# Kernel optimization log

Measured on AMD Instinct MI355X. Metric: run time of the kernel, lower is better.

The kernel has to match this reference:

```python
import jax, jax.numpy as jnp
import numpy as np

CLIP = 100000.0


def heaviside(x):
    # smooth heaviside surrogate used by the layer
    return (jnp.tanh(10.0 * x) + 1.0) * 0.5


def evapotranspiration(wu, wl, wd, pet):
    et1 = heaviside(wu - pet) * pet + heaviside(pet - wu) * wu
    rem = heaviside(0.0 - (pet - et1)) * 0.0 + heaviside(pet - et1) * (pet - et1)
    et22 = heaviside(rem - wl) * wl + heaviside(wl - rem) * rem
    et2 = heaviside(rem) * et22
    et33 = heaviside(rem - et2 - wd) * wd + heaviside(wd - (rem - et2)) * (rem - et2)
    et3 = heaviside(rem - et2) * et33
    return et1, et2, et3


def runoff_production(wu, wl, wd, p, wum, wlm, wdm, b, c):
    wum = wum * 19.9 + 0.1
    wlm = wlm * 30.0 + 60.0
    wdm = wdm * 60.0 + 60.0
    c = c * 0.19 + 0.01
    b = b * 0.3 + 0.1
    w_total = wum + wlm + wdm
    s = c * (wu / w_total) ** 2 + b * (wl / w_total) ** 2
    return heaviside(p - s) * (p - s)


def water_source_partition(runoff, k1, k2, k3):
    k1 = k1 * 0.69 + 0.01
    k2 = k2 * 0.69 + 0.01
    k3 = k3 * 0.89 + 0.01
    surface = k1 * runoff
    interflow = k2 * (runoff - surface)
    baseflow = k3 * (runoff - surface - interflow)
    return surface, interflow, baseflow


def flow_routing(surface, interflow, baseflow):
    return surface + 0.5 * interflow + 0.25 * baseflow


def xaj_forward(inputs, wum, wlm, wdm, c, b, k1, k2, k3):
    # inputs: (B, T, 3) channels = [pet, tmean, p]
    pet_seq = inputs[:, :, 0:1]
    p_seq = inputs[:, :, 2:3]

    B = inputs.shape[0]
    # time-major driver: (T, B, 2) = [pet, p] per step (tmean unused in step)
    xs = jnp.moveaxis(jnp.stack([inputs[:, :, 0], inputs[:, :, 2]], axis=-1), 1, 0)

    def step(state, xt):
        # state: (B, 3) = [wu, wl, wd]; xt: (B, 2) = [pet, p]
        wu, wl, wd = state[:, 0], state[:, 1], state[:, 2]
        pet, p = xt[:, 0], xt[:, 1]
        et1, et2, et3 = evapotranspiration(wu, wl, wd, pet)
        wu_n = wu + jnp.clip(p - et1, -CLIP, CLIP)
        wl_n = wl + jnp.clip(p - et1 - et2, -CLIP, CLIP)
        wd_n = wd + jnp.clip(p - et1 - et2 - et3, -CLIP, CLIP)
        ns = jnp.stack([wu_n, wl_n, wd_n], axis=1)
        return ns, ns

    init = jnp.zeros((B, 3), dtype=inputs.dtype)
    _, traj = jax.lax.scan(step, init, xs)           # (T, B, 3)
    outputs = jnp.moveaxis(traj, 0, 1)               # (B, T, 3)

    wu = outputs[:, :, 0:1]
    wl = outputs[:, :, 1:2]
    wd = outputs[:, :, 2:3]

    # NOTE: original call site passes (wu, wd, wl, ...) and (wum, wdm, wlm, ...)
    # positionally into runoff_production -- replicated faithfully.
    runoff = runoff_production(wu, wd, wl, p_seq, wum, wdm, wlm, b, c)
    surface, interflow, baseflow = water_source_partition(runoff, k1, k2, k3)
    total_q = flow_routing(surface, interflow, baseflow)  # (B, T, 1)
    return total_q


def setup_inputs() -> dict:
    key = jax.random.key(0)
    ks = jax.random.split(key, 9)
    B, T = 4096, 2048
    inp = {"inputs": jax.random.uniform(ks[0], (B, T, 3), dtype=jnp.float32)}
    for i, name in enumerate(["wum", "wlm", "wdm", "c", "b", "k1", "k2", "k3"]):
        inp[name] = jax.random.uniform(ks[i + 1], (1,), dtype=jnp.float32)
    return inp


def reference(inputs, wum, wlm, wdm, c, b, k1, k2, k3):
    return xaj_forward(inputs, wum, wlm, wdm, c, b, k1, k2, k3)
```

## Files before the change

### kernel.cpp

```cpp
#include <hip/hip_runtime.h>

typedef float  f32x4 __attribute__((ext_vector_type(4)));
typedef __fp16 f16x2 __attribute__((ext_vector_type(2)));

#define T_LEN 2048
#define GROUP 32
#define NG    (T_LEN / GROUP)
#define NT    (NG + 3)
#define KH    28.853901f

__device__ __forceinline__ float hs_neg(float z) {
    float e = __builtin_amdgcn_exp2f(z);
    return __builtin_amdgcn_rcpf(1.0f + e);
}

#define WAITV(N) asm volatile("s_waitcnt vmcnt(" #N ")" ::: "memory")
#define WAITL()  asm volatile("s_waitcnt lgkmcnt(0)" ::: "memory")
#define TICK_BARRIER() do {                                   \
    asm volatile("s_waitcnt lgkmcnt(0)" ::: "memory");        \
    __builtin_amdgcn_s_barrier();                             \
    __builtin_amdgcn_sched_barrier(0); } while (0)

#define DMA_CHUNK(SLOT, C) do {                                                \
    const float* g_ = row + (size_t)(C) * 48;                                  \
    _Pragma("unroll")                                                          \
    for (int j_ = 0; j_ < 12; ++j_) {                                          \
        __builtin_amdgcn_global_load_lds(                                      \
            (const __attribute__((address_space(1))) void*)(g_ + 4 * j_),      \
            (__attribute__((address_space(3))) void*)&s_in[SLOT][j_][0],       \
            16, 0, 0);                                                         \
    } } while (0)

__global__ __launch_bounds__(256, 1)
void xaj_k32_kernel(const float* __restrict__ inp,
                    const float* __restrict__ p_wum,
                    const float* __restrict__ p_wlm,
                    const float* __restrict__ p_wdm,
                    const float* __restrict__ p_c,
                    const float* __restrict__ p_b,
                    const float* __restrict__ p_k1,
                    const float* __restrict__ p_k2,
                    const float* __restrict__ p_k3,
                    float* __restrict__ out)
{
    __shared__ f32x4        s_in  [3][12][64];
    __shared__ float        s_krem[2][GROUP][64];
    __shared__ float        s_kd1 [2][GROUP][64];
    __shared__ float        s_ku  [2][GROUP][64];
    __shared__ float        s_kd2 [2][GROUP][64];
    __shared__ float        s_kwd [2][GROUP][64];
    __shared__ unsigned int s_wup [4][GROUP][64];

    const int lane  = threadIdx.x & 63;
    const int wv    = threadIdx.x >> 6;
    const int chain = blockIdx.x * 64 + lane;
    const float* __restrict__ row = inp + (size_t)chain * (3 * T_LEN);
    float* __restrict__ orow      = out + (size_t)chain * T_LEN;

    const float wum = p_wum[0], wlm = p_wlm[0], wdm = p_wdm[0];
    const float cc  = p_c[0],   bb  = p_b[0];
    const float k1  = p_k1[0],  k2  = p_k2[0],  k3 = p_k3[0];

    const float w_total = (wum * 19.9f + 0.1f)
                        + (wdm * 30.0f + 60.0f)
                        + (wlm * 60.0f + 60.0f);
    const float inv_wt = 1.0f / w_total;
    const float c_s = cc * 0.19f + 0.01f;
    const float b_s = bb * 0.3f  + 0.1f;
    const float k1s = k1 * 0.69f + 0.01f;
    const float k2s = k2 * 0.69f + 0.01f;
    const float k3s = k3 * 0.89f + 0.01f;
    const float Kq = k1s + 0.5f * k2s * (1.0f - k1s)
                   + 0.25f * k3s * (1.0f - k1s) * (1.0f - k2s);
    const float C1 = inv_wt / KH;

    float Kst = 0.0f;
    int s0 = 0, s1 = 1, s2 = 2;

    if (wv == 0) { DMA_CHUNK(0, 0); DMA_CHUNK(1, 1); }

#pragma clang loop unroll(disable)
    for (int T = 0; T < NT; ++T) {
        if (wv == 0) {
            if (T < NG) {
                const int g = T;
                WAITV(0);
                f32x4 fv[24];
#pragma unroll
                for (int j = 0; j < 12; ++j) fv[j]      = s_in[s0][j][lane];
#pragma unroll
                for (int j = 0; j < 12; ++j) fv[12 + j] = s_in[s1][j][lane];
                WAITL();
                __builtin_amdgcn_sched_barrier(0);
                const int c2 = 2 * g + 2, c3 = 2 * g + 3;
                if (c2 < 2 * NG) DMA_CHUNK(s2, c2);
                if (c3 < 2 * NG) DMA_CHUNK(s0, c3);
                float Kwu = Kst;
#pragma unroll
                for (int j = 0; j < GROUP; ++j) {
                    const int k0 = 3 * j, k2i = 3 * j + 2;
                    float pet = fv[k0 >> 2][k0 & 3];
                    float p   = fv[k2i >> 2][k2i & 3];
                    float KHpet = KH * pet, Kp = KH * p;
                    float arg  = KHpet - Kwu;
                    float a    = hs_neg(arg);
                    float Kwun = fmaf(-arg, a, Kp);
                    float Kd1  = Kwun - Kwu;
                    float Ky   = arg + (Kwun - Kp);
                    float hx   = hs_neg(-Ky);
                    float Krem = hx * Ky;
                    s_krem[g & 1][j][lane] = Krem;
                    s_kd1 [g & 1][j][lane] = Kd1;
                    f16x2 pk = __builtin_amdgcn_cvt_pkrtz(Kwun, p);
                    s_wup[g & 3][j][lane] = __builtin_bit_cast(unsigned int, pk);
                    Kwu = Kwun;
                }
                Kst = Kwu;
                int t0 = s0; s0 = s2; s2 = s1; s1 = t0;
            }
        } else if (wv == 1) {
            if (T >= 1 && T <= NG) {
                const int g = T - 1;
                float Kwl = Kst;
#pragma unroll
                for (int j = 0; j < GROUP; ++j) {
                    float Krem = s_krem[g & 1][j][lane];
                    float Kd1  = s_kd1 [g & 1][j][lane];
                    float hrem = hs_neg(-Krem);
                    float S    = Kwl + Kd1;
                    float A    = fmaf(-hrem, Krem, S);
                    float arg  = Kwl - Krem;
                    float b2   = hs_neg(arg);
                    float harg = hrem * arg;
                    float Kwln = fmaf(-b2, harg, A);
                    float Ket2 = S - Kwln;
                    s_ku [g & 1][j][lane] = Krem - Ket2;
                    s_kd2[g & 1][j][lane] = Kd1 - Ket2;
                    Kwl = Kwln;
                }
                Kst = Kwl;
            }
        } else if (wv == 2) {
            if (T >= 2 && T <= NG + 1) {
                const int g = T - 2;
                float Kwd = Kst;
#pragma unroll
                for (int j = 0; j < GROUP; ++j) {
                    float Ku  = s_ku [g & 1][j][lane];
                    float Kd2 = s_kd2[g & 1][j][lane];
                    float hu  = hs_neg(-Ku);
                    float S2  = Kwd + Kd2;
                    float A2  = fmaf(-hu, Ku, S2);
                    float arg = Kwd - Ku;
                    float c2v = hs_neg(arg);
                    float harg = hu * arg;
                    float Kwdn = fmaf(-c2v, harg, A2);
                    s_kwd[g & 1][j][lane] = Kwdn;
                    Kwd = Kwdn;
                }
                Kst = Kwd;
            }
        } else {
            if (T >= 3) {
                const int g = T - 3;
                float qv[GROUP];
#pragma unroll
                for (int j = 0; j < GROUP; ++j) {
                    unsigned int pw = s_wup[g & 3][j][lane];
                    f16x2 pk = __builtin_bit_cast(f16x2, pw);
                    float Kwu_ = (float)pk[0];
                    float p    = (float)pk[1];
                    float Kwd_ = s_kwd[g & 1][j][lane];
                    float ru = Kwu_ * C1;
                    float rd = Kwd_ * C1;
                    float s2v = fmaf(c_s * ru, ru, (b_s * rd) * rd);
                    float ps = p - s2v;
                    float so = hs_neg(-KH * ps);
                    qv[j] = ps * so * Kq;
                }
                f32x4* o4 = (f32x4*)(orow + (size_t)g * GROUP);
#pragma unroll
                for (int i = 0; i < GROUP / 4; ++i) {
                    f32x4 q = {qv[4*i], qv[4*i+1], qv[4*i+2], qv[4*i+3]};
                    o4[i] = q;
                }
            }
        }
        TICK_BARRIER();
    }
}

extern "C" void kernel_launch(void* const* d_in, const int* in_sizes, int n_in,
                              void* d_out, int out_size, void* d_ws, size_t ws_size,
                              hipStream_t stream) {
    const float* inp = (const float*)d_in[0];
    const int B = out_size / T_LEN;
    dim3 block(256), grid(B / 64);
    xaj_k32_kernel<<<grid, block, 0, stream>>>(
        inp,
        (const float*)d_in[1],
        (const float*)d_in[2],
        (const float*)d_in[3],
        (const float*)d_in[4],
        (const float*)d_in[5],
        (const float*)d_in[6],
        (const float*)d_in[7],
        (const float*)d_in[8],
        (float*)d_out);
}
```

Baseline: 134.4 us.

## Run two 4-wave stage pipelines per block with smaller groups and fp16 wd handoff

Each 512-thread block now holds two independent 4-wave pipelines, each serving 64 chains, so there are half as many blocks. The time group shrinks from 32 to 16 steps and the input prefetch is simplified to a double buffer. The wd trajectory handed to the output wave is stored in fp16 to save LDS. The aim is more chains resident per CU and better latency hiding across the serial recurrence stages. The cost is twice as many barrier ticks, fewer blocks across the GPU, and reduced precision on the stored wd value.

```diff
diff --git a/kernel.cpp b/kernel.cpp
--- a/kernel.cpp
+++ b/kernel.cpp
@@ -4,7 +4,7 @@
 typedef __fp16 f16x2 __attribute__((ext_vector_type(2)));
 
 #define T_LEN 2048
-#define GROUP 32
+#define GROUP 16
 #define NG    (T_LEN / GROUP)
 #define NT    (NG + 3)
 #define KH    28.853901f
@@ -21,39 +21,41 @@
     __builtin_amdgcn_s_barrier();                             \
     __builtin_amdgcn_sched_barrier(0); } while (0)
 
-#define DMA_CHUNK(SLOT, C) do {                                                \
-    const float* g_ = row + (size_t)(C) * 48;                                  \
+#define DMA_GROUP(PIPE, SLOT, G) do {                                          \
+    const float* g_ = row + (size_t)(G) * 48;                                  \
     _Pragma("unroll")                                                          \
     for (int j_ = 0; j_ < 12; ++j_) {                                          \
         __builtin_amdgcn_global_load_lds(                                      \
             (const __attribute__((address_space(1))) void*)(g_ + 4 * j_),      \
-            (__attribute__((address_space(3))) void*)&s_in[SLOT][j_][0],       \
+            (__attribute__((address_space(3))) void*)&s_in[PIPE][SLOT][j_][0], \
             16, 0, 0);                                                         \
     } } while (0)
 
-__global__ __launch_bounds__(256, 1)
-void xaj_k32_kernel(const float* __restrict__ inp,
-                    const float* __restrict__ p_wum,
-                    const float* __restrict__ p_wlm,
-                    const float* __restrict__ p_wdm,
-                    const float* __restrict__ p_c,
-                    const float* __restrict__ p_b,
-                    const float* __restrict__ p_k1,
-                    const float* __restrict__ p_k2,
-                    const float* __restrict__ p_k3,
-                    float* __restrict__ out)
+__global__ __launch_bounds__(512, 1)
+void xaj_dual_kernel(const float* __restrict__ inp,
+                     const float* __restrict__ p_wum,
+                     const float* __restrict__ p_wlm,
+                     const float* __restrict__ p_wdm,
+                     const float* __restrict__ p_c,
+                     const float* __restrict__ p_b,
+                     const float* __restrict__ p_k1,
+                     const float* __restrict__ p_k2,
+                     const float* __restrict__ p_k3,
+                     float* __restrict__ out)
 {
-    __shared__ f32x4        s_in  [3][12][64];
-    __shared__ float        s_krem[2][GROUP][64];
-    __shared__ float        s_kd1 [2][GROUP][64];
-    __shared__ float        s_ku  [2][GROUP][64];
-    __shared__ float        s_kd2 [2][GROUP][64];
-    __shared__ float        s_kwd [2][GROUP][64];
-    __shared__ unsigned int s_wup [4][GROUP][64];
+    __shared__ f32x4        s_in  [2][2][12][64];
+    __shared__ float        s_krem[2][2][GROUP][64];
+    __shared__ float        s_kd1 [2][2][GROUP][64];
+    __shared__ float        s_ku  [2][2][GROUP][64];
+    __shared__ float        s_kd2 [2][2][GROUP][64];
+    __shared__ __fp16       s_kwd [2][2][GROUP][64];
+    __shared__ unsigned int s_wup [2][4][GROUP][64];
 
     const int lane  = threadIdx.x & 63;
     const int wv    = threadIdx.x >> 6;
-    const int chain = blockIdx.x * 64 + lane;
+    const int pipe  = wv >> 2;
+    const int stage = wv & 3;
+    const int chain = blockIdx.x * 128 + pipe * 64 + lane;
     const float* __restrict__ row = inp + (size_t)chain * (3 * T_LEN);
     float* __restrict__ orow      = out + (size_t)chain * T_LEN;
 
@@ -75,26 +77,21 @@
     const float C1 = inv_wt / KH;
 
     float Kst = 0.0f;
-    int s0 = 0, s1 = 1, s2 = 2;
-
-    if (wv == 0) { DMA_CHUNK(0, 0); DMA_CHUNK(1, 1); }
+
+    if (stage == 0) DMA_GROUP(pipe, 0, 0);
 
 #pragma clang loop unroll(disable)
     for (int T = 0; T < NT; ++T) {
-        if (wv == 0) {
+        if (stage == 0) {
             if (T < NG) {
                 const int g = T;
                 WAITV(0);
-                f32x4 fv[24];
-#pragma unroll
-                for (int j = 0; j < 12; ++j) fv[j]      = s_in[s0][j][lane];
-#pragma unroll
-                for (int j = 0; j < 12; ++j) fv[12 + j] = s_in[s1][j][lane];
+                f32x4 fv[12];
+#pragma unroll
+                for (int j = 0; j < 12; ++j) fv[j] = s_in[pipe][g & 1][j][lane];
                 WAITL();
                 __builtin_amdgcn_sched_barrier(0);
-                const int c2 = 2 * g + 2, c3 = 2 * g + 3;
-                if (c2 < 2 * NG) DMA_CHUNK(s2, c2);
-                if (c3 < 2 * NG) DMA_CHUNK(s0, c3);
+                if (g + 1 < NG) DMA_GROUP(pipe, (g + 1) & 1, g + 1);
                 float Kwu = Kst;
 #pragma unroll
                 for (int j = 0; j < GROUP; ++j) {
@@ -109,23 +106,23 @@
                     float Ky   = arg + (Kwun - Kp);
                     float hx   = hs_neg(-Ky);
                     float Krem = hx * Ky;
-                    s_krem[g & 1][j][lane] = Krem;
-                    s_kd1 [g & 1][j][lane] = Kd1;
+                    s_krem[pipe][g & 1][j][lane] = Krem;
+                    s_kd1 [pipe][g & 1][j][lane] = Kd1;
                     f16x2 pk = __builtin_amdgcn_cvt_pkrtz(Kwun, p);
-                    s_wup[g & 3][j][lane] = __builtin_bit_cast(unsigned int, pk);
+                    s_wup[pipe][g & 3][j][lane] =
+                        __builtin_bit_cast(unsigned int, pk);
                     Kwu = Kwun;
                 }
                 Kst = Kwu;
-                int t0 = s0; s0 = s2; s2 = s1; s1 = t0;
-            }
-        } else if (wv == 1) {
+            }
+        } else if (stage == 1) {
             if (T >= 1 && T <= NG) {
                 const int g = T - 1;
                 float Kwl = Kst;
 #pragma unroll
                 for (int j = 0; j < GROUP; ++j) {
-                    float Krem = s_krem[g & 1][j][lane];
-                    float Kd1  = s_kd1 [g & 1][j][lane];
+                    float Krem = s_krem[pipe][g & 1][j][lane];
+                    float Kd1  = s_kd1 [pipe][g & 1][j][lane];
                     float hrem = hs_neg(-Krem);
                     float S    = Kwl + Kd1;
                     float A    = fmaf(-hrem, Krem, S);
@@ -134,20 +131,20 @@
                     float harg = hrem * arg;
                     float Kwln = fmaf(-b2, harg, A);
                     float Ket2 = S - Kwln;
-                    s_ku [g & 1][j][lane] = Krem - Ket2;
-                    s_kd2[g & 1][j][lane] = Kd1 - Ket2;
+                    s_ku [pipe][g & 1][j][lane] = Krem - Ket2;
+                    s_kd2[pipe][g & 1][j][lane] = Kd1 - Ket2;
                     Kwl = Kwln;
                 }
                 Kst = Kwl;
             }
-        } else if (wv == 2) {
+        } else if (stage == 2) {
             if (T >= 2 && T <= NG + 1) {
                 const int g = T - 2;
                 float Kwd = Kst;
 #pragma unroll
                 for (int j = 0; j < GROUP; ++j) {
-                    float Ku  = s_ku [g & 1][j][lane];
-                    float Kd2 = s_kd2[g & 1][j][lane];
+                    float Ku  = s_ku [pipe][g & 1][j][lane];
+                    float Kd2 = s_kd2[pipe][g & 1][j][lane];
                     float hu  = hs_neg(-Ku);
                     float S2  = Kwd + Kd2;
                     float A2  = fmaf(-hu, Ku, S2);
@@ -155,7 +152,7 @@
                     float c2v = hs_neg(arg);
                     float harg = hu * arg;
                     float Kwdn = fmaf(-c2v, harg, A2);
-                    s_kwd[g & 1][j][lane] = Kwdn;
+                    s_kwd[pipe][g & 1][j][lane] = (__fp16)Kwdn;
                     Kwd = Kwdn;
                 }
                 Kst = Kwd;
@@ -166,11 +163,11 @@
                 float qv[GROUP];
 #pragma unroll
                 for (int j = 0; j < GROUP; ++j) {
-                    unsigned int pw = s_wup[g & 3][j][lane];
+                    unsigned int pw = s_wup[pipe][g & 3][j][lane];
                     f16x2 pk = __builtin_bit_cast(f16x2, pw);
                     float Kwu_ = (float)pk[0];
                     float p    = (float)pk[1];
-                    float Kwd_ = s_kwd[g & 1][j][lane];
+                    float Kwd_ = (float)s_kwd[pipe][g & 1][j][lane];
                     float ru = Kwu_ * C1;
                     float rd = Kwd_ * C1;
                     float s2v = fmaf(c_s * ru, ru, (b_s * rd) * rd);
@@ -195,8 +192,8 @@
                               hipStream_t stream) {
     const float* inp = (const float*)d_in[0];
     const int B = out_size / T_LEN;
-    dim3 block(256), grid(B / 64);
-    xaj_k32_kernel<<<grid, block, 0, stream>>>(
+    dim3 block(512), grid(B / 128);
+    xaj_dual_kernel<<<grid, block, 0, stream>>>(
         inp,
         (const float*)d_in[1],
         (const float*)d_in[2],
```

After: 202.3 us. 50.5% more time.

## Move input loading to the output wave and halve the group size

Applied to the files above, without the earlier changes.

Input DMA and unpacking move from the first recurrence wave to the fourth (output) wave, which pre-scales pet and p into a shared buffer one group ahead. This keeps the serial wave-0 chain free of load latency. Group size drops from 32 to 16, doubling the number of barrier ticks but shortening each pipeline stage. Pairs of intermediates are packed into float2 LDS stores, and the deep-store value is kept in fp16, which costs precision in the runoff computation.

```diff
diff --git a/kernel.cpp b/kernel.cpp
--- a/kernel.cpp
+++ b/kernel.cpp
@@ -1,10 +1,11 @@
 #include <hip/hip_runtime.h>
 
+typedef float  f32x2 __attribute__((ext_vector_type(2)));
 typedef float  f32x4 __attribute__((ext_vector_type(4)));
 typedef __fp16 f16x2 __attribute__((ext_vector_type(2)));
 
 #define T_LEN 2048
-#define GROUP 32
+#define GROUP 16
 #define NG    (T_LEN / GROUP)
 #define NT    (NG + 3)
 #define KH    28.853901f
@@ -15,14 +16,13 @@
 }
 
 #define WAITV(N) asm volatile("s_waitcnt vmcnt(" #N ")" ::: "memory")
-#define WAITL()  asm volatile("s_waitcnt lgkmcnt(0)" ::: "memory")
 #define TICK_BARRIER() do {                                   \
     asm volatile("s_waitcnt lgkmcnt(0)" ::: "memory");        \
     __builtin_amdgcn_s_barrier();                             \
     __builtin_amdgcn_sched_barrier(0); } while (0)
 
-#define DMA_CHUNK(SLOT, C) do {                                                \
-    const float* g_ = row + (size_t)(C) * 48;                                  \
+#define DMA_GROUP(SLOT, G) do {                                                \
+    const float* g_ = row + (size_t)(G) * 48;                                  \
     _Pragma("unroll")                                                          \
     for (int j_ = 0; j_ < 12; ++j_) {                                          \
         __builtin_amdgcn_global_load_lds(                                      \
@@ -32,7 +32,7 @@
     } } while (0)
 
 __global__ __launch_bounds__(256, 1)
-void xaj_k32_kernel(const float* __restrict__ inp,
+void xaj_bal_kernel(const float* __restrict__ inp,
                     const float* __restrict__ p_wum,
                     const float* __restrict__ p_wlm,
                     const float* __restrict__ p_wdm,
@@ -43,13 +43,12 @@
                     const float* __restrict__ p_k3,
                     float* __restrict__ out)
 {
-    __shared__ f32x4        s_in  [3][12][64];
-    __shared__ float        s_krem[2][GROUP][64];
-    __shared__ float        s_kd1 [2][GROUP][64];
-    __shared__ float        s_ku  [2][GROUP][64];
-    __shared__ float        s_kd2 [2][GROUP][64];
-    __shared__ float        s_kwd [2][GROUP][64];
-    __shared__ unsigned int s_wup [4][GROUP][64];
+    __shared__ f32x4        s_in    [3][12][64];
+    __shared__ f32x2        s_pp    [2][GROUP][64];
+    __shared__ f32x2        s_kremd1[2][GROUP][64];
+    __shared__ f32x2        s_kud2  [2][GROUP][64];
+    __shared__ __fp16       s_kwd   [2][GROUP][64];
+    __shared__ unsigned int s_wup   [4][GROUP][64];
 
     const int lane  = threadIdx.x & 63;
     const int wv    = threadIdx.x >> 6;
@@ -72,36 +71,41 @@
     const float k3s = k3 * 0.89f + 0.01f;
     const float Kq = k1s + 0.5f * k2s * (1.0f - k1s)
                    + 0.25f * k3s * (1.0f - k1s) * (1.0f - k2s);
-    const float C1 = inv_wt / KH;
+    const float C1    = inv_wt / KH;
+    const float invKH = 1.0f / KH;
 
     float Kst = 0.0f;
-    int s0 = 0, s1 = 1, s2 = 2;
-
-    if (wv == 0) { DMA_CHUNK(0, 0); DMA_CHUNK(1, 1); }
+
+    if (wv == 3) {
+        DMA_GROUP(0, 0);
+        DMA_GROUP(1, 1);
+        WAITV(12);
+        __builtin_amdgcn_sched_barrier(0);
+        f32x4 fv[12];
+#pragma unroll
+        for (int j = 0; j < 12; ++j) fv[j] = s_in[0][j][lane];
+#pragma unroll
+        for (int j = 0; j < GROUP; ++j) {
+            const int k0 = 3 * j, k2i = 3 * j + 2;
+            f32x2 pp = {KH * fv[k0 >> 2][k0 & 3], KH * fv[k2i >> 2][k2i & 3]};
+            s_pp[0][j][lane] = pp;
+        }
+        DMA_GROUP(2, 2);
+    }
+    TICK_BARRIER();
 
 #pragma clang loop unroll(disable)
     for (int T = 0; T < NT; ++T) {
         if (wv == 0) {
             if (T < NG) {
                 const int g = T;
-                WAITV(0);
-                f32x4 fv[24];
-#pragma unroll
-                for (int j = 0; j < 12; ++j) fv[j]      = s_in[s0][j][lane];
-#pragma unroll
-                for (int j = 0; j < 12; ++j) fv[12 + j] = s_in[s1][j][lane];
-                WAITL();
-                __builtin_amdgcn_sched_barrier(0);
-                const int c2 = 2 * g + 2, c3 = 2 * g + 3;
-                if (c2 < 2 * NG) DMA_CHUNK(s2, c2);
-                if (c3 < 2 * NG) DMA_CHUNK(s0, c3);
+                f32x2 ppv[GROUP];
+#pragma unroll
+                for (int j = 0; j < GROUP; ++j) ppv[j] = s_pp[g & 1][j][lane];
                 float Kwu = Kst;
 #pragma unroll
                 for (int j = 0; j < GROUP; ++j) {
-                    const int k0 = 3 * j, k2i = 3 * j + 2;
-                    float pet = fv[k0 >> 2][k0 & 3];
-                    float p   = fv[k2i >> 2][k2i & 3];
-                    float KHpet = KH * pet, Kp = KH * p;
+                    float KHpet = ppv[j][0], Kp = ppv[j][1];
                     float arg  = KHpet - Kwu;
                     float a    = hs_neg(arg);
                     float Kwun = fmaf(-arg, a, Kp);
@@ -109,23 +113,24 @@
                     float Ky   = arg + (Kwun - Kp);
                     float hx   = hs_neg(-Ky);
                     float Krem = hx * Ky;
-                    s_krem[g & 1][j][lane] = Krem;
-                    s_kd1 [g & 1][j][lane] = Kd1;
-                    f16x2 pk = __builtin_amdgcn_cvt_pkrtz(Kwun, p);
+                    f32x2 kd = {Krem, Kd1};
+                    s_kremd1[g & 1][j][lane] = kd;
+                    f16x2 pk = __builtin_amdgcn_cvt_pkrtz(Kwun, Kp);
                     s_wup[g & 3][j][lane] = __builtin_bit_cast(unsigned int, pk);
                     Kwu = Kwun;
                 }
                 Kst = Kwu;
-                int t0 = s0; s0 = s2; s2 = s1; s1 = t0;
             }
         } else if (wv == 1) {
             if (T >= 1 && T <= NG) {
                 const int g = T - 1;
+                f32x2 kd[GROUP];
+#pragma unroll
+                for (int j = 0; j < GROUP; ++j) kd[j] = s_kremd1[g & 1][j][lane];
                 float Kwl = Kst;
 #pragma unroll
                 for (int j = 0; j < GROUP; ++j) {
-                    float Krem = s_krem[g & 1][j][lane];
-                    float Kd1  = s_kd1 [g & 1][j][lane];
+                    float Krem = kd[j][0], Kd1 = kd[j][1];
                     float hrem = hs_neg(-Krem);
                     float S    = Kwl + Kd1;
                     float A    = fmaf(-hrem, Krem, S);
@@ -134,8 +139,8 @@
                     float harg = hrem * arg;
                     float Kwln = fmaf(-b2, harg, A);
                     float Ket2 = S - Kwln;
-                    s_ku [g & 1][j][lane] = Krem - Ket2;
-                    s_kd2[g & 1][j][lane] = Kd1 - Ket2;
+                    f32x2 ud = {Krem - Ket2, Kd1 - Ket2};
+                    s_kud2[g & 1][j][lane] = ud;
                     Kwl = Kwln;
                 }
                 Kst = Kwl;
@@ -143,11 +148,13 @@
         } else if (wv == 2) {
             if (T >= 2 && T <= NG + 1) {
                 const int g = T - 2;
+                f32x2 ud[GROUP];
+#pragma unroll
+                for (int j = 0; j < GROUP; ++j) ud[j] = s_kud2[g & 1][j][lane];
                 float Kwd = Kst;
 #pragma unroll
                 for (int j = 0; j < GROUP; ++j) {
-                    float Ku  = s_ku [g & 1][j][lane];
-                    float Kd2 = s_kd2[g & 1][j][lane];
+                    float Ku = ud[j][0], Kd2 = ud[j][1];
                     float hu  = hs_neg(-Ku);
                     float S2  = Kwd + Kd2;
                     float A2  = fmaf(-hu, Ku, S2);
@@ -155,12 +162,28 @@
                     float c2v = hs_neg(arg);
                     float harg = hu * arg;
                     float Kwdn = fmaf(-c2v, harg, A2);
-                    s_kwd[g & 1][j][lane] = Kwdn;
+                    s_kwd[g & 1][j][lane] = (__fp16)Kwdn;
                     Kwd = Kwdn;
                 }
                 Kst = Kwd;
             }
         } else {
+            if (T + 1 < NG) {
+                WAITV(12);
+                __builtin_amdgcn_sched_barrier(0);
+                const int gp = T + 1;
+                f32x4 fv[12];
+#pragma unroll
+                for (int j = 0; j < 12; ++j) fv[j] = s_in[gp % 3][j][lane];
+#pragma unroll
+                for (int j = 0; j < GROUP; ++j) {
+                    const int k0 = 3 * j, k2i = 3 * j + 2;
+                    f32x2 pp = {KH * fv[k0 >> 2][k0 & 3],
+                                KH * fv[k2i >> 2][k2i & 3]};
+                    s_pp[gp & 1][j][lane] = pp;
+                }
+                if (T + 3 < NG) DMA_GROUP((T + 3) % 3, T + 3);
+            }
             if (T >= 3) {
                 const int g = T - 3;
                 float qv[GROUP];
@@ -169,8 +192,8 @@
                     unsigned int pw = s_wup[g & 3][j][lane];
                     f16x2 pk = __builtin_bit_cast(f16x2, pw);
                     float Kwu_ = (float)pk[0];
-                    float p    = (float)pk[1];
-                    float Kwd_ = s_kwd[g & 1][j][lane];
+                    float p    = (float)pk[1] * invKH;
+                    float Kwd_ = (float)s_kwd[g & 1][j][lane];
                     float ru = Kwu_ * C1;
                     float rd = Kwd_ * C1;
                     float s2v = fmaf(c_s * ru, ru, (b_s * rd) * rd);
@@ -196,7 +219,7 @@
     const float* inp = (const float*)d_in[0];
     const int B = out_size / T_LEN;
     dim3 block(256), grid(B / 64);
-    xaj_k32_kernel<<<grid, block, 0, stream>>>(
+    xaj_bal_kernel<<<grid, block, 0, stream>>>(
         inp,
         (const float*)d_in[1],
         (const float*)d_in[2],
```

Result: slower. 148.9 us (+10.8%).

## Process two chains per lane with interleaved recurrences and halved group size

Applied to the files above, without the earlier changes.

Each lane now advances two independent batch chains (A and B) through every pipeline stage. The goal is to interleave their serial exp/rcp dependency chains for instruction-level parallelism, so the grid shrinks to half as many blocks. The group length drops from 32 to 16 to fit the doubled register and LDS buffers, which doubles the number of block barriers. Stage-to-stage LDS traffic is packed into float2 pairs, and the deep-store state and scaled precipitation now pass through fp16. That adds rounding risk on large storage values and leaves fewer blocks to cover the GPU's compute units.

```diff
diff --git a/kernel.cpp b/kernel.cpp
--- a/kernel.cpp
+++ b/kernel.cpp
@@ -1,10 +1,11 @@
 #include <hip/hip_runtime.h>
 
+typedef float  f32x2 __attribute__((ext_vector_type(2)));
 typedef float  f32x4 __attribute__((ext_vector_type(4)));
 typedef __fp16 f16x2 __attribute__((ext_vector_type(2)));
 
 #define T_LEN 2048
-#define GROUP 32
+#define GROUP 16
 #define NG    (T_LEN / GROUP)
 #define NT    (NG + 3)
 #define KH    28.853901f
@@ -21,41 +22,42 @@
     __builtin_amdgcn_s_barrier();                             \
     __builtin_amdgcn_sched_barrier(0); } while (0)
 
-#define DMA_CHUNK(SLOT, C) do {                                                \
-    const float* g_ = row + (size_t)(C) * 48;                                  \
+#define DMA_GROUP(SET, SLOT, ROW, G) do {                                      \
+    const float* g_ = (ROW) + (size_t)(G) * 48;                                \
     _Pragma("unroll")                                                          \
     for (int j_ = 0; j_ < 12; ++j_) {                                          \
         __builtin_amdgcn_global_load_lds(                                      \
             (const __attribute__((address_space(1))) void*)(g_ + 4 * j_),      \
-            (__attribute__((address_space(3))) void*)&s_in[SLOT][j_][0],       \
+            (__attribute__((address_space(3))) void*)&s_in[SET][SLOT][j_][0],  \
             16, 0, 0);                                                         \
     } } while (0)
 
 __global__ __launch_bounds__(256, 1)
-void xaj_k32_kernel(const float* __restrict__ inp,
-                    const float* __restrict__ p_wum,
-                    const float* __restrict__ p_wlm,
-                    const float* __restrict__ p_wdm,
-                    const float* __restrict__ p_c,
-                    const float* __restrict__ p_b,
-                    const float* __restrict__ p_k1,
-                    const float* __restrict__ p_k2,
-                    const float* __restrict__ p_k3,
-                    float* __restrict__ out)
+void xaj_ilp2_kernel(const float* __restrict__ inp,
+                     const float* __restrict__ p_wum,
+                     const float* __restrict__ p_wlm,
+                     const float* __restrict__ p_wdm,
+                     const float* __restrict__ p_c,
+                     const float* __restrict__ p_b,
+                     const float* __restrict__ p_k1,
+                     const float* __restrict__ p_k2,
+                     const float* __restrict__ p_k3,
+                     float* __restrict__ out)
 {
-    __shared__ f32x4        s_in  [3][12][64];
-    __shared__ float        s_krem[2][GROUP][64];
-    __shared__ float        s_kd1 [2][GROUP][64];
-    __shared__ float        s_ku  [2][GROUP][64];
-    __shared__ float        s_kd2 [2][GROUP][64];
-    __shared__ float        s_kwd [2][GROUP][64];
-    __shared__ unsigned int s_wup [4][GROUP][64];
+    __shared__ f32x4        s_in    [2][2][12][64];
+    __shared__ f32x2        s_kremd1[2][2][GROUP][64];
+    __shared__ f32x2        s_kud2  [2][2][GROUP][64];
+    __shared__ __fp16       s_kwd   [2][2][GROUP][64];
+    __shared__ unsigned int s_wup   [2][4][GROUP][64];
 
     const int lane  = threadIdx.x & 63;
     const int wv    = threadIdx.x >> 6;
-    const int chain = blockIdx.x * 64 + lane;
-    const float* __restrict__ row = inp + (size_t)chain * (3 * T_LEN);
-    float* __restrict__ orow      = out + (size_t)chain * T_LEN;
+    const int cA    = blockIdx.x * 128 + lane;
+    const int cB    = cA + 64;
+    const float* __restrict__ rowA = inp + (size_t)cA * (3 * T_LEN);
+    const float* __restrict__ rowB = inp + (size_t)cB * (3 * T_LEN);
+    float* __restrict__ orowA      = out + (size_t)cA * T_LEN;
+    float* __restrict__ orowB      = out + (size_t)cB * T_LEN;
 
     const float wum = p_wum[0], wlm = p_wlm[0], wdm = p_wdm[0];
     const float cc  = p_c[0],   bb  = p_b[0];
@@ -72,12 +74,12 @@
     const float k3s = k3 * 0.89f + 0.01f;
     const float Kq = k1s + 0.5f * k2s * (1.0f - k1s)
                    + 0.25f * k3s * (1.0f - k1s) * (1.0f - k2s);
-    const float C1 = inv_wt / KH;
-
-    float Kst = 0.0f;
-    int s0 = 0, s1 = 1, s2 = 2;
-
-    if (wv == 0) { DMA_CHUNK(0, 0); DMA_CHUNK(1, 1); }
+    const float C1    = inv_wt / KH;
+    const float invKH = 1.0f / KH;
+
+    float KstA = 0.0f, KstB = 0.0f;
+
+    if (wv == 0) { DMA_GROUP(0, 0, rowA, 0); DMA_GROUP(1, 0, rowB, 0); }
 
 #pragma clang loop unroll(disable)
     for (int T = 0; T < NT; ++T) {
@@ -85,104 +87,137 @@
             if (T < NG) {
                 const int g = T;
                 WAITV(0);
-                f32x4 fv[24];
-#pragma unroll
-                for (int j = 0; j < 12; ++j) fv[j]      = s_in[s0][j][lane];
-#pragma unroll
-                for (int j = 0; j < 12; ++j) fv[12 + j] = s_in[s1][j][lane];
+                __builtin_amdgcn_sched_barrier(0);
+                f32x4 fa[12], fb[12];
+#pragma unroll
+                for (int j = 0; j < 12; ++j) fa[j] = s_in[0][g & 1][j][lane];
+#pragma unroll
+                for (int j = 0; j < 12; ++j) fb[j] = s_in[1][g & 1][j][lane];
                 WAITL();
                 __builtin_amdgcn_sched_barrier(0);
-                const int c2 = 2 * g + 2, c3 = 2 * g + 3;
-                if (c2 < 2 * NG) DMA_CHUNK(s2, c2);
-                if (c3 < 2 * NG) DMA_CHUNK(s0, c3);
-                float Kwu = Kst;
+                if (g + 1 < NG) {
+                    DMA_GROUP(0, (g + 1) & 1, rowA, g + 1);
+                    DMA_GROUP(1, (g + 1) & 1, rowB, g + 1);
+                }
+                float KwuA = KstA, KwuB = KstB;
 #pragma unroll
                 for (int j = 0; j < GROUP; ++j) {
                     const int k0 = 3 * j, k2i = 3 * j + 2;
-                    float pet = fv[k0 >> 2][k0 & 3];
-                    float p   = fv[k2i >> 2][k2i & 3];
-                    float KHpet = KH * pet, Kp = KH * p;
-                    float arg  = KHpet - Kwu;
-                    float a    = hs_neg(arg);
-                    float Kwun = fmaf(-arg, a, Kp);
-                    float Kd1  = Kwun - Kwu;
-                    float Ky   = arg + (Kwun - Kp);
-                    float hx   = hs_neg(-Ky);
-                    float Krem = hx * Ky;
-                    s_krem[g & 1][j][lane] = Krem;
-                    s_kd1 [g & 1][j][lane] = Kd1;
-                    f16x2 pk = __builtin_amdgcn_cvt_pkrtz(Kwun, p);
-                    s_wup[g & 3][j][lane] = __builtin_bit_cast(unsigned int, pk);
-                    Kwu = Kwun;
-                }
-                Kst = Kwu;
-                int t0 = s0; s0 = s2; s2 = s1; s1 = t0;
+                    float petA = fa[k0 >> 2][k0 & 3], pA = fa[k2i >> 2][k2i & 3];
+                    float petB = fb[k0 >> 2][k0 & 3], pB = fb[k2i >> 2][k2i & 3];
+                    float KpA = KH * pA, KpB = KH * pB;
+                    float argA = fmaf(KH, petA, -KwuA);
+                    float argB = fmaf(KH, petB, -KwuB);
+                    float aA = hs_neg(argA), aB = hs_neg(argB);
+                    float KwuAn = fmaf(-argA, aA, KpA);
+                    float KwuBn = fmaf(-argB, aB, KpB);
+                    float KyA = argA + (KwuAn - KpA);
+                    float KyB = argB + (KwuBn - KpB);
+                    float hxA = hs_neg(-KyA), hxB = hs_neg(-KyB);
+                    f32x2 kdA = {hxA * KyA, KwuAn - KwuA};
+                    f32x2 kdB = {hxB * KyB, KwuBn - KwuB};
+                    s_kremd1[0][g & 1][j][lane] = kdA;
+                    s_kremd1[1][g & 1][j][lane] = kdB;
+                    f16x2 pkA = __builtin_amdgcn_cvt_pkrtz(KwuAn, KpA);
+                    f16x2 pkB = __builtin_amdgcn_cvt_pkrtz(KwuBn, KpB);
+                    s_wup[0][g & 3][j][lane] = __builtin_bit_cast(unsigned int, pkA);
+                    s_wup[1][g & 3][j][lane] = __builtin_bit_cast(unsigned int, pkB);
+                    KwuA = KwuAn; KwuB = KwuBn;
+                }
+                KstA = KwuA; KstB = KwuB;
             }
         } else if (wv == 1) {
             if (T >= 1 && T <= NG) {
                 const int g = T - 1;
-                float Kwl = Kst;
-#pragma unroll
-                for (int j = 0; j < GROUP; ++j) {
-                    float Krem = s_krem[g & 1][j][lane];
-                    float Kd1  = s_kd1 [g & 1][j][lane];
-                    float hrem = hs_neg(-Krem);
-                    float S    = Kwl + Kd1;
-                    float A    = fmaf(-hrem, Krem, S);
-                    float arg  = Kwl - Krem;
-                    float b2   = hs_neg(arg);
-                    float harg = hrem * arg;
-                    float Kwln = fmaf(-b2, harg, A);
-                    float Ket2 = S - Kwln;
-                    s_ku [g & 1][j][lane] = Krem - Ket2;
-                    s_kd2[g & 1][j][lane] = Kd1 - Ket2;
-                    Kwl = Kwln;
-                }
-                Kst = Kwl;
+                f32x2 kdA[GROUP], kdB[GROUP];
+#pragma unroll
+                for (int j = 0; j < GROUP; ++j) {
+                    kdA[j] = s_kremd1[0][g & 1][j][lane];
+                    kdB[j] = s_kremd1[1][g & 1][j][lane];
+                }
+                float KwlA = KstA, KwlB = KstB;
+#pragma unroll
+                for (int j = 0; j < GROUP; ++j) {
+                    float KremA = kdA[j][0], Kd1A = kdA[j][1];
+                    float KremB = kdB[j][0], Kd1B = kdB[j][1];
+                    float hremA = hs_neg(-KremA), hremB = hs_neg(-KremB);
+                    float SA = KwlA + Kd1A,     SB = KwlB + Kd1B;
+                    float AA = fmaf(-hremA, KremA, SA);
+                    float AB = fmaf(-hremB, KremB, SB);
+                    float argA = KwlA - KremA,  argB = KwlB - KremB;
+                    float b2A = hs_neg(argA),   b2B = hs_neg(argB);
+                    float hargA = hremA * argA, hargB = hremB * argB;
+                    float KwlAn = fmaf(-b2A, hargA, AA);
+                    float KwlBn = fmaf(-b2B, hargB, AB);
+                    float Ket2A = SA - KwlAn,   Ket2B = SB - KwlBn;
+                    f32x2 udA = {KremA - Ket2A, Kd1A - Ket2A};
+                    f32x2 udB = {KremB - Ket2B, Kd1B - Ket2B};
+                    s_kud2[0][g & 1][j][lane] = udA;
+                    s_kud2[1][g & 1][j][lane] = udB;
+                    KwlA = KwlAn; KwlB = KwlBn;
+                }
+                KstA = KwlA; KstB = KwlB;
             }
         } else if (wv == 2) {
             if (T >= 2 && T <= NG + 1) {
                 const int g = T - 2;
-                float Kwd = Kst;
-#pragma unroll
-                for (int j = 0; j < GROUP; ++j) {
-                    float Ku  = s_ku [g & 1][j][lane];
-                    float Kd2 = s_kd2[g & 1][j][lane];
-                    float hu  = hs_neg(-Ku);
-                    float S2  = Kwd + Kd2;
-                    float A2  = fmaf(-hu, Ku, S2);
-                    float arg = Kwd - Ku;
-                    float c2v = hs_neg(arg);
-                    float harg = hu * arg;
-                    float Kwdn = fmaf(-c2v, harg, A2);
-                    s_kwd[g & 1][j][lane] = Kwdn;
-                    Kwd = Kwdn;
-                }
-                Kst = Kwd;
+                f32x2 udA[GROUP], udB[GROUP];
+#pragma unroll
+                for (int j = 0; j < GROUP; ++j) {
+                    udA[j] = s_kud2[0][g & 1][j][lane];
+                    udB[j] = s_kud2[1][g & 1][j][lane];
+                }
+                float KwdA = KstA, KwdB = KstB;
+#pragma unroll
+                for (int j = 0; j < GROUP; ++j) {
+                    float KuA = udA[j][0], Kd2A = udA[j][1];
+                    float KuB = udB[j][0], Kd2B = udB[j][1];
+                    float huA = hs_neg(-KuA), huB = hs_neg(-KuB);
+                    float S2A = KwdA + Kd2A,  S2B = KwdB + Kd2B;
+                    float A2A = fmaf(-huA, KuA, S2A);
+                    float A2B = fmaf(-huB, KuB, S2B);
+                    float argA = KwdA - KuA,  argB = KwdB - KuB;
+                    float c2A = hs_neg(argA), c2B = hs_neg(argB);
+                    float hargA = huA * argA, hargB = huB * argB;
+                    float KwdAn = fmaf(-c2A, hargA, A2A);
+                    float KwdBn = fmaf(-c2B, hargB, A2B);
+                    s_kwd[0][g & 1][j][lane] = (__fp16)KwdAn;
+                    s_kwd[1][g & 1][j][lane] = (__fp16)KwdBn;
+                    KwdA = KwdAn; KwdB = KwdBn;
+                }
+                KstA = KwdA; KstB = KwdB;
             }
         } else {
             if (T >= 3) {
                 const int g = T - 3;
-                float qv[GROUP];
-#pragma unroll
-                for (int j = 0; j < GROUP; ++j) {
-                    unsigned int pw = s_wup[g & 3][j][lane];
-                    f16x2 pk = __builtin_bit_cast(f16x2, pw);
-                    float Kwu_ = (float)pk[0];
-                    float p    = (float)pk[1];
-                    float Kwd_ = s_kwd[g & 1][j][lane];
-                    float ru = Kwu_ * C1;
-                    float rd = Kwd_ * C1;
-                    float s2v = fmaf(c_s * ru, ru, (b_s * rd) * rd);
-                    float ps = p - s2v;
-                    float so = hs_neg(-KH * ps);
-                    qv[j] = ps * so * Kq;
-                }
-                f32x4* o4 = (f32x4*)(orow + (size_t)g * GROUP);
+                float qvA[GROUP], qvB[GROUP];
+#pragma unroll
+                for (int j = 0; j < GROUP; ++j) {
+                    unsigned int pwA = s_wup[0][g & 3][j][lane];
+                    unsigned int pwB = s_wup[1][g & 3][j][lane];
+                    f16x2 pkA = __builtin_bit_cast(f16x2, pwA);
+                    f16x2 pkB = __builtin_bit_cast(f16x2, pwB);
+                    float KwuA_ = (float)pkA[0], pAv = (float)pkA[1] * invKH;
+                    float KwuB_ = (float)pkB[0], pBv = (float)pkB[1] * invKH;
+                    float KwdA_ = (float)s_kwd[0][g & 1][j][lane];
+                    float KwdB_ = (float)s_kwd[1][g & 1][j][lane];
+                    float ruA = KwuA_ * C1, rdA = KwdA_ * C1;
+                    float ruB = KwuB_ * C1, rdB = KwdB_ * C1;
+                    float s2A = fmaf(c_s * ruA, ruA, (b_s * rdA) * rdA);
+                    float s2B = fmaf(c_s * ruB, ruB, (b_s * rdB) * rdB);
+                    float psA = pAv - s2A, psB = pBv - s2B;
+                    float soA = hs_neg(-KH * psA), soB = hs_neg(-KH * psB);
+                    qvA[j] = psA * soA * Kq;
+                    qvB[j] = psB * soB * Kq;
+                }
+                f32x4* oA = (f32x4*)(orowA + (size_t)g * GROUP);
+                f32x4* oB = (f32x4*)(orowB + (size_t)g * GROUP);
 #pragma unroll
                 for (int i = 0; i < GROUP / 4; ++i) {
-                    f32x4 q = {qv[4*i], qv[4*i+1], qv[4*i+2], qv[4*i+3]};
-                    o4[i] = q;
+                    f32x4 qa = {qvA[4*i], qvA[4*i+1], qvA[4*i+2], qvA[4*i+3]};
+                    f32x4 qb = {qvB[4*i], qvB[4*i+1], qvB[4*i+2], qvB[4*i+3]};
+                    oA[i] = qa;
+                    oB[i] = qb;
                 }
             }
         }
@@ -195,8 +230,8 @@
                               hipStream_t stream) {
     const float* inp = (const float*)d_in[0];
     const int B = out_size / T_LEN;
-    dim3 block(256), grid(B / 64);
-    xaj_k32_kernel<<<grid, block, 0, stream>>>(
+    dim3 block(256), grid(B / 128);
+    xaj_ilp2_kernel<<<grid, block, 0, stream>>>(
         inp,
         (const float*)d_in[1],
         (const float*)d_in[2],
```

Result: slower. 233.2 us (+73.5%).
